# Optimization experiments

Measured on AMD Instinct MI355X. Metric: run time of the kernel, lower is better.

The kernel has to match this reference:

```python
import jax, jax.numpy as jnp
import numpy as np

D_MODEL = 528
N_HEADS = 16
FEAT = 16           # feature_dim
HEAD_DIM = 33       # d_model // num_heads == 2*FEAT + 1 (required by the module's math)
WINDOW = 64
EPS = 1e-9


def setup_inputs() -> dict:
    key = jax.random.key(0)
    ks = jax.random.split(key, 10)
    B, S = 2, 2048
    hidden_states = jax.random.normal(ks[0], (B, S, D_MODEL), dtype=jnp.float32)
    attention_mask = jnp.ones((B, S), dtype=jnp.int32)
    sc = 0.02
    # weights stored as (in, out); torch Linear applies x @ W.T so this is the transposed weight
    Wq_lin = jax.random.normal(ks[1], (D_MODEL, FEAT * N_HEADS), dtype=jnp.float32) * sc
    Wk_lin = jax.random.normal(ks[2], (D_MODEL, FEAT * N_HEADS), dtype=jnp.float32) * sc
    Wv_lin = jax.random.normal(ks[3], (D_MODEL, HEAD_DIM * N_HEADS), dtype=jnp.float32) * sc
    Wo_lin = jax.random.normal(ks[4], (HEAD_DIM * N_HEADS, D_MODEL), dtype=jnp.float32) * sc
    Wq_win = jax.random.normal(ks[5], (D_MODEL, D_MODEL), dtype=jnp.float32) * sc
    Wk_win = jax.random.normal(ks[6], (D_MODEL, D_MODEL), dtype=jnp.float32) * sc
    Wv_win = jax.random.normal(ks[7], (D_MODEL, D_MODEL), dtype=jnp.float32) * sc
    Wo_win = jax.random.normal(ks[8], (D_MODEL, D_MODEL), dtype=jnp.float32) * sc
    return {
        "hidden_states": hidden_states,
        "attention_mask": attention_mask,
        "Wq_lin": Wq_lin, "Wk_lin": Wk_lin, "Wv_lin": Wv_lin, "Wo_lin": Wo_lin,
        "Wq_win": Wq_win, "Wk_win": Wk_win, "Wv_win": Wv_win, "Wo_win": Wo_win,
    }


def _linear_attention(x, mask, Wq, Wk, Wv, Wo):
    B, S, _ = x.shape
    q = (x @ Wq).reshape(B, S, N_HEADS, FEAT).transpose(0, 2, 1, 3)      # bhsf
    k = (x @ Wk).reshape(B, S, N_HEADS, FEAT).transpose(0, 2, 1, 3)
    v = (x @ Wv).reshape(B, S, N_HEADS, HEAD_DIM).transpose(0, 2, 1, 3)  # bhse
    # Taylor feature map: [1, q, 0.5*q^2] -> feature dim 2*FEAT+1 == HEAD_DIM
    qe = jnp.concatenate([jnp.ones_like(q[..., :1]), q, 0.5 * q * q], axis=-1)
    ke = jnp.concatenate([jnp.ones_like(k[..., :1]), k, 0.5 * k * k], axis=-1)
    kv = jnp.einsum('bhnd,bhne->bhde', ke, v)          # (B,H,Dexp,HEAD_DIM)
    qkv = jnp.einsum('bhnd,bhde->bhne', qe, kv)        # (B,H,S,HEAD_DIM)
    # z[b,h,n,e] = (sum_d qe[b,h,n,d]) * ksum[b,h,e]  (faithful to torch einsum with size-1 n)
    z = qe.sum(-1, keepdims=True) * ke.sum(2, keepdims=True)  # (B,H,S,Dexp==HEAD_DIM)
    out = qkv / (z + EPS)
    out = jnp.where((mask == 0)[:, None, :, None], 0.0, out)
    out = out.transpose(0, 2, 1, 3).reshape(B, S, N_HEADS * HEAD_DIM)
    return out @ Wo


def _window_attention(x, mask, Wq, Wk, Wv, Wo):
    B, S, _ = x.shape
    q = (x @ Wq).reshape(B, S, N_HEADS, HEAD_DIM).transpose(0, 2, 1, 3)
    k = (x @ Wk).reshape(B, S, N_HEADS, HEAD_DIM).transpose(0, 2, 1, 3)
    v = (x @ Wv).reshape(B, S, N_HEADS, HEAD_DIM).transpose(0, 2, 1, 3)
    scores = jnp.einsum('bhnd,bhmd->bhnm', q, k) / np.sqrt(HEAD_DIM).astype(np.float32)
    # tril(diagonal=window_size-1): allow key index m <= n + WINDOW - 1
    i = jnp.arange(S)[:, None]
    j = jnp.arange(S)[None, :]
    band = (j <= i + WINDOW - 1)
    neg_inf = jnp.asarray(-jnp.inf, scores.dtype)
    scores = jnp.where(band[None, None], scores, neg_inf)
    scores = jnp.where((mask == 0)[:, None, None, :], neg_inf, scores)
    attn = jax.nn.softmax(scores, axis=-1)
    out = jnp.einsum('bhnm,bhmd->bhnd', attn, v)
    out = out.transpose(0, 2, 1, 3).reshape(B, S, D_MODEL)
    return out @ Wo


def reference(hidden_states, attention_mask,
              Wq_lin, Wk_lin, Wv_lin, Wo_lin,
              Wq_win, Wk_win, Wv_win, Wo_win):
    lin = _linear_attention(hidden_states, attention_mask, Wq_lin, Wk_lin, Wv_lin, Wo_lin)
    win = _window_attention(hidden_states, attention_mask, Wq_win, Wk_win, Wv_win, Wo_win)
    return lin + win
```

## Files before the change

### kernel.cpp

```cpp
#include <hip/hip_runtime.h>

#define NH 16
#define FEAT 16
#define HD 33
#define DM 528
#define WIN 64
#define EPSF 1e-9f
#define K1C (0.17407765595569785f * 1.4426950408889634f)
#define KP 544
#define KSPLIT 1632
#define NPROJ 2112
#define KOUT 1056
#define OPS 4352
#define NCH 16
#define ZPARTS 4

typedef float f32x4 __attribute__((ext_vector_type(4)));
typedef short short8 __attribute__((ext_vector_type(8)));

__device__ inline ushort f2bf(float f) {
  uint u = __float_as_uint(f);
  uint r = u + 0x7fffu + ((u >> 16) & 1u);
  return (ushort)(r >> 16);
}
__device__ inline ushort f2bf_tr(float f) { return (ushort)(__float_as_uint(f) >> 16); }
__device__ inline float bf2f(ushort u) { return __uint_as_float(((uint)u) << 16); }

__global__ __launch_bounds__(256) void prep_all(const float* __restrict__ x,
                                                const float* __restrict__ Wq_lin,
                                                const float* __restrict__ Wk_lin,
                                                const float* __restrict__ Wv_lin,
                                                const float* __restrict__ Wo_lin,
                                                const float* __restrict__ Wq_win,
                                                const float* __restrict__ Wk_win,
                                                const float* __restrict__ Wv_win,
                                                const float* __restrict__ Wo_win,
                                                ushort* __restrict__ xhi,
                                                ushort* __restrict__ xlo,
                                                ushort* __restrict__ Wqks,
                                                ushort* __restrict__ WprojT,
                                                ushort* __restrict__ WoT2, int M) {
  const int stride = gridDim.x * 256;
  const int tid0 = blockIdx.x * 256 + threadIdx.x;
  for (int j = tid0; j < M * 68; j += stride) {
    int row = j / 68, c8 = (j - row * 68) * 8;
    short8 h8, l8;
    if (c8 < DM) {
      float4 f0 = *(const float4*)&x[(size_t)row * DM + c8];
      float4 f1 = *(const float4*)&x[(size_t)row * DM + c8 + 4];
      float vv[8] = {f0.x, f0.y, f0.z, f0.w, f1.x, f1.y, f1.z, f1.w};
#pragma unroll
      for (int z = 0; z < 8; ++z) {
        ushort h = f2bf(vv[z]);
        h8[z] = (short)h;
        l8[z] = (short)f2bf(vv[z] - bf2f(h));
      }
    } else {
      h8 = (short8){0, 0, 0, 0, 0, 0, 0, 0};
      l8 = h8;
    }
    *(short8*)&xhi[(size_t)row * KP + c8] = h8;
    *(short8*)&xlo[(size_t)row * KP + c8] = l8;
  }
  for (int i = tid0; i < 512 * KSPLIT; i += stride) {
    int n = i / KSPLIT, kp = i - n * KSPLIT;
    int seg = kp / KP, kk = kp - seg * KP;
    float v = 0.f;
    if (kk < DM) v = (n < 256) ? Wq_lin[(size_t)kk * 256 + n] : Wk_lin[(size_t)kk * 256 + (n - 256)];
    ushort h = f2bf(v);
    if (seg == 2) h = f2bf(v - bf2f(h));
    Wqks[i] = h;
  }
  for (int i = tid0; i < NPROJ * KP; i += stride) {
    int n = i / KP, k = i - n * KP;
    float v = 0.f;
    if (k < DM) {
      if (n < DM) v = Wq_win[(size_t)k * DM + n];
      else if (n < 2 * DM) v = Wk_win[(size_t)k * DM + (n - DM)] * K1C;
      else if (n < 3 * DM) v = Wv_win[(size_t)k * DM + (n - 2 * DM)];
      else v = Wv_lin[(size_t)k * DM + (n - 3 * DM)];
    }
    WprojT[i] = f2bf(v);
  }
  for (int i = tid0; i < DM * KOUT; i += stride) {
    int n = i / KOUT, k = i - n * KOUT;
    float v = (k < DM) ? Wo_lin[(size_t)k * DM + n] : Wo_win[(size_t)(k - DM) * DM + n];
    WoT2[i] = f2bf(v);
  }
}

__global__ __launch_bounds__(256) void proj_fused(const ushort* __restrict__ xhi,
                                                  const ushort* __restrict__ xlo,
                                                  const ushort* __restrict__ Wqks,
                                                  const ushort* __restrict__ WprojT,
                                                  float* __restrict__ qk,
                                                  ushort* __restrict__ qkvw,
                                                  float* __restrict__ v_lin,
                                                  const int* __restrict__ maskp,
                                                  int S) {
  __shared__ ushort As[128][36];
  __shared__ ushort Bs[128][36];
  const int bm = blockIdx.x * 128;
  const int tid = threadIdx.x;
  const int lane = tid & 63, w = tid >> 6;
  const int lo = lane & 15, hi = lane >> 4;
  const int wr = w >> 1, wc = w & 1;
  const short8 zv = {0, 0, 0, 0, 0, 0, 0, 0};
  f32x4 acc[4][4];
#pragma unroll
  for (int mb = 0; mb < 4; ++mb)
#pragma unroll
    for (int nb = 0; nb < 4; ++nb) acc[mb][nb] = (f32x4){0.f, 0.f, 0.f, 0.f};

  if (blockIdx.y < 17) {
    const int bn = blockIdx.y * 128;
    for (int k0 = 0; k0 < KP; k0 += 32) {
      short8 a_ld[2], b_ld[2];
#pragma unroll
      for (int p = 0; p < 2; ++p) {
        int c = tid + p * 256;
        int row = c >> 2, cc = c & 3;
        a_ld[p] = *(const short8*)&xhi[(size_t)(bm + row) * KP + k0 + cc * 8];
        int bnr = bn + row;
        b_ld[p] = (bnr < NPROJ) ? *(const short8*)&WprojT[(size_t)bnr * KP + k0 + cc * 8] : zv;
      }
      __syncthreads();
#pragma unroll
      for (int p = 0; p < 2; ++p) {
        int c = tid + p * 256;
        int row = c >> 2, cc = c & 3;
        *(short8*)&As[row][cc * 8] = a_ld[p];
        *(short8*)&Bs[row][cc * 8] = b_ld[p];
      }
      __syncthreads();
      short8 afr[4], bfr[4];
#pragma unroll
      for (int mb = 0; mb < 4; ++mb) afr[mb] = *(const short8*)&As[wr * 64 + 16 * mb + lo][8 * hi];
#pragma unroll
      for (int nb = 0; nb < 4; ++nb) bfr[nb] = *(const short8*)&Bs[wc * 64 + 16 * nb + lo][8 * hi];
#pragma unroll
      for (int mb = 0; mb < 4; ++mb)
#pragma unroll
        for (int nb = 0; nb < 4; ++nb)
          acc[mb][nb] = __builtin_amdgcn_mfma_f32_16x16x32_bf16(afr[mb], bfr[nb], acc[mb][nb], 0, 0, 0);
    }
#pragma unroll
    for (int nb = 0; nb < 4; ++nb) {
      const int col = bn + wc * 64 + 16 * nb + lo;
      if (col >= NPROJ) continue;
      const int seg = col / DM;
      const int cc = col - seg * DM;
      if (seg == 3) {
#pragma unroll
        for (int mb = 0; mb < 4; ++mb)
#pragma unroll
          for (int r = 0; r < 4; ++r) {
            int row = bm + wr * 64 + 16 * mb + 4 * hi + r;
            v_lin[(size_t)row * DM + cc] = acc[mb][nb][r];
          }
      } else {
        const uint h = ((uint)cc * 993u) >> 15;
        const int e = cc - (int)h * 33;
        ushort* dst = qkvw + (size_t)seg * (32u * (uint)S * 40u);
#pragma unroll
        for (int mb = 0; mb < 4; ++mb)
#pragma unroll
          for (int r = 0; r < 4; ++r) {
            int row = bm + wr * 64 + 16 * mb + 4 * hi + r;
            int b = (row >= S) ? 1 : 0;
            int nn = row - b * S;
            float val = acc[mb][nb][r];
            if (seg == 2) {
              size_t tb = (size_t)(b * NH + (int)h) * 40;
              dst[(tb + e) * S + nn] = f2bf(val);
              if (e == 0) {
                dst[(tb + 33) * S + nn] = 0x3F80;
#pragma unroll
                for (int z = 34; z < 40; ++z) dst[(tb + z) * S + nn] = 0;
              }
            } else {
              size_t base = ((size_t)(b * NH + (int)h) * S + nn) * 40;
              dst[base + e] = f2bf(val);
              if (e == 0) {
                ushort pad33 = (seg == 0) ? (ushort)0x3F80
                                          : (maskp[row] ? (ushort)0 : f2bf(-1e30f));
                dst[base + 33] = pad33;
#pragma unroll
                for (int z = 34; z < 40; ++z) dst[base + z] = 0;
              }
            }
          }
      }
    }
  } else {
    const int bn = (blockIdx.y - 17) * 128;
    for (int k0 = 0; k0 < KSPLIT; k0 += 32) {
      const int seg = k0 / KP;
      const int kk = k0 - seg * KP;
      const ushort* xsrc = (seg == 1) ? xlo : xhi;
      short8 a_ld[2], b_ld[2];
#pragma unroll
      for (int p = 0; p < 2; ++p) {
        int c = tid + p * 256;
        int row = c >> 2, cc = c & 3;
        a_ld[p] = *(const short8*)&xsrc[(size_t)(bm + row) * KP + kk + cc * 8];
        b_ld[p] = *(const short8*)&Wqks[(size_t)(bn + row) * KSPLIT + k0 + cc * 8];
      }
      __syncthreads();
#pragma unroll
      for (int p = 0; p < 2; ++p) {
        int c = tid + p * 256;
        int row = c >> 2, cc = c & 3;
        *(short8*)&As[row][cc * 8] = a_ld[p];
        *(short8*)&Bs[row][cc * 8] = b_ld[p];
      }
      __syncthreads();
      short8 afr[4], bfr[4];
#pragma unroll
      for (int mb = 0; mb < 4; ++mb) afr[mb] = *(const short8*)&As[wr * 64 + 16 * mb + lo][8 * hi];
#pragma unroll
      for (int nb = 0; nb < 4; ++nb) bfr[nb] = *(const short8*)&Bs[wc * 64 + 16 * nb + lo][8 * hi];
#pragma unroll
      for (int mb = 0; mb < 4; ++mb)
#pragma unroll
        for (int nb = 0; nb < 4; ++nb)
          acc[mb][nb] = __builtin_amdgcn_mfma_f32_16x16x32_bf16(afr[mb], bfr[nb], acc[mb][nb], 0, 0, 0);
    }
#pragma unroll
    for (int mb = 0; mb < 4; ++mb)
#pragma unroll
      for (int nb = 0; nb < 4; ++nb) {
        int col = bn + wc * 64 + 16 * nb + lo;
#pragma unroll
        for (int r = 0; r < 4; ++r) {
          int row = bm + wr * 64 + 16 * mb + 4 * hi + r;
          qk[(size_t)row * 512 + col] = acc[mb][nb][r];
        }
      }
  }
}

__global__ __launch_bounds__(256) void gemm_out(const ushort* __restrict__ A,
                                                const ushort* __restrict__ Bt,
                                                float* __restrict__ C, int S) {
  __shared__ ushort As[128][36];
  __shared__ ushort Bs[128][36];
  const int bm = blockIdx.x * 128, bn = blockIdx.y * 128;
  const int tid = threadIdx.x;
  const int lane = tid & 63, w = tid >> 6;
  const int lo = lane & 15, hi = lane >> 4;
  const int wr = w >> 1, wc = w & 1;
  f32x4 acc[4][4];
#pragma unroll
  for (int mb = 0; mb < 4; ++mb)
#pragma unroll
    for (int nb = 0; nb < 4; ++nb) acc[mb][nb] = (f32x4){0.f, 0.f, 0.f, 0.f};
  const short8 zv = {0, 0, 0, 0, 0, 0, 0, 0};

  for (int k0 = 0; k0 < KOUT; k0 += 32) {
    short8 a_ld[2], b_ld[2];
#pragma unroll
    for (int p = 0; p < 2; ++p) {
      int c = tid + p * 256;
      int row = c >> 2, cc = c & 3;
      a_ld[p] = *(const short8*)&A[(size_t)(bm + row) * KOUT + k0 + cc * 8];
      int bnr = bn + row;
      b_ld[p] = (bnr < DM) ? *(const short8*)&Bt[(size_t)bnr * KOUT + k0 + cc * 8] : zv;
    }
    __syncthreads();
#pragma unroll
    for (int p = 0; p < 2; ++p) {
      int c = tid + p * 256;
      int row = c >> 2, cc = c & 3;
      *(short8*)&As[row][cc * 8] = a_ld[p];
      *(short8*)&Bs[row][cc * 8] = b_ld[p];
    }
    __syncthreads();
    short8 afr[4], bfr[4];
#pragma unroll
    for (int mb = 0; mb < 4; ++mb) afr[mb] = *(const short8*)&As[wr * 64 + 16 * mb + lo][8 * hi];
#pragma unroll
    for (int nb = 0; nb < 4; ++nb) bfr[nb] = *(const short8*)&Bs[wc * 64 + 16 * nb + lo][8 * hi];
#pragma unroll
    for (int mb = 0; mb < 4; ++mb)
#pragma unroll
      for (int nb = 0; nb < 4; ++nb)
        acc[mb][nb] = __builtin_amdgcn_mfma_f32_16x16x32_bf16(afr[mb], bfr[nb], acc[mb][nb], 0, 0, 0);
  }
#pragma unroll
  for (int nb = 0; nb < 4; ++nb) {
    const int col = bn + wc * 64 + 16 * nb + lo;
    if (col >= DM) continue;
#pragma unroll
    for (int mb = 0; mb < 4; ++mb)
#pragma unroll
      for (int r = 0; r < 4; ++r) {
        int row = bm + wr * 64 + 16 * mb + 4 * hi + r;
        C[(size_t)row * DM + col] = acc[mb][nb][r];
      }
  }
}

__global__ __launch_bounds__(256) void lin_red(const float* __restrict__ kvp,
                                               float* __restrict__ kvr) {
  int bh = blockIdx.x;
  for (int i = threadIdx.x; i < 1188; i += 256) {
    float s = 0.f;
#pragma unroll
    for (int c = 0; c < NCH; ++c) s += kvp[(size_t)(bh * NCH + c) * 1188 + i];
    kvr[(size_t)bh * 1188 + i] = s;
  }
}

__global__ __launch_bounds__(256) void win_kv(const ushort* __restrict__ qwb,
                                              const ushort* __restrict__ kwb,
                                              const ushort* __restrict__ vwbT,
                                              ushort* __restrict__ Opart,
                                              const float* __restrict__ qk,
                                              const float* __restrict__ v_lin,
                                              float* __restrict__ kvp,
                                              int B, int S, int NT2) {
  __shared__ ushort sh[4][32][72];
  const int tid = threadIdx.x;
  const int NWINBLK = NT2 * 32 * ZPARTS;
  const int bx = blockIdx.x;

  if (bx < NWINBLK) {
    const int bh = bx & 31;
    const int qp = bx >> 5;
    const int part = qp / NT2;
    const int qt = NT2 - 1 - (qp - part * NT2);
    const int NT = NT2 * 2;
    const int T = min(NT, 2 * qt + 3);
    if (part >= T) return;
    const int n0 = qt * 128;
    const int lane = tid & 63, w = tid >> 6;
    const int lo = lane & 15, hi = lane >> 4;
    const short8 zv = {0, 0, 0, 0, 0, 0, 0, 0};
    ushort (*Ps)[32][72] = sh;

    short8 qf[2][2];
#pragma unroll
    for (int qr = 0; qr < 2; ++qr) {
      const ushort* qrow = qwb + ((size_t)bh * S + n0 + w * 32 + qr * 16 + lo) * 40;
      qf[qr][0] = *(const short8*)&qrow[8 * hi];
      qf[qr][1] = (hi == 0) ? *(const short8*)&qrow[32] : zv;
    }

    const ushort* kb = kwb + (size_t)bh * S * 40;
    const ushort* vb = vwbT + (size_t)bh * 40 * S;
    int evc[3];
#pragma unroll
    for (int eb = 0; eb < 3; ++eb) {
      int e = 16 * eb + lo;
      evc[eb] = (e > 39) ? 39 : e;
    }

    f32x4 Oacc[2][3];
#pragma unroll
    for (int qr = 0; qr < 2; ++qr)
#pragma unroll
      for (int eb = 0; eb < 3; ++eb) Oacc[qr][eb] = (f32x4){0.f, 0.f, 0.f, 0.f};

    for (int t = part; t < T; t += ZPARTS) {
      const int m0 = t * 64;
      short8 kf0[4], kf1[4];
#pragma unroll
      for (int bb = 0; bb < 4; ++bb) {
        const ushort* kr = kb + (size_t)(m0 + 16 * bb + lo) * 40;
        kf0[bb] = *(const short8*)&kr[8 * hi];
        kf1[bb] = *(const short8*)&kr[32];
      }
      short8 vf0[3], vf1[3];
#pragma unroll
      for (int eb = 0; eb < 3; ++eb) {
        const ushort* vr = vb + (size_t)evc[eb] * S + m0;
        vf0[eb] = *(const short8*)&vr[8 * hi];
        vf1[eb] = *(const short8*)&vr[32 + 8 * hi];
      }

      f32x4 accS[2][4];
#pragma unroll
      for (int qr = 0; qr < 2; ++qr)
#pragma unroll
        for (int bb = 0; bb < 4; ++bb) accS[qr][bb] = (f32x4){0.f, 0.f, 0.f, 0.f};
      __builtin_amdgcn_s_setprio(1);
#pragma unroll
      for (int bb = 0; bb < 4; ++bb)
#pragma unroll
        for (int qr = 0; qr < 2; ++qr) {
          accS[qr][bb] = __builtin_amdgcn_mfma_f32_16x16x32_bf16(qf[qr][0], kf0[bb], accS[qr][bb], 0, 0, 0);
          accS[qr][bb] = __builtin_amdgcn_mfma_f32_16x16x32_bf16(qf[qr][1], kf1[bb], accS[qr][bb], 0, 0, 0);
        }
      __builtin_amdgcn_s_setprio(0);

      const bool boundary = (m0 > n0);
      const int dmn = m0 - n0;
#pragma unroll
      for (int qr = 0; qr < 2; ++qr)
#pragma unroll
        for (int bb = 0; bb < 4; ++bb)
#pragma unroll
          for (int r = 0; r < 4; ++r) {
            float p = exp2f(accS[qr][bb][r]);
            if (boundary) {
              int rr = w * 32 + qr * 16 + 4 * hi + r;
              int c = 16 * bb + lo;
              if (c > rr + 63 - dmn) p = 0.f;
            }
            Ps[w][qr * 16 + 4 * hi + r][16 * bb + lo] = f2bf_tr(p);
          }

      __builtin_amdgcn_s_setprio(1);
#pragma unroll
      for (int qr = 0; qr < 2; ++qr) {
        short8 pf0 = *(const short8*)&Ps[w][qr * 16 + lo][8 * hi];
        short8 pf1 = *(const short8*)&Ps[w][qr * 16 + lo][32 + 8 * hi];
#pragma unroll
        for (int eb = 0; eb < 3; ++eb) {
          Oacc[qr][eb] = __builtin_amdgcn_mfma_f32_16x16x32_bf16(pf0, vf0[eb], Oacc[qr][eb], 0, 0, 0);
          Oacc[qr][eb] = __builtin_amdgcn_mfma_f32_16x16x32_bf16(pf1, vf1[eb], Oacc[qr][eb], 0, 0, 0);
        }
      }
      __builtin_amdgcn_s_setprio(0);
    }

    const size_t ob = ((size_t)(bh * NT2 + qt) * ZPARTS + part) * OPS;
#pragma unroll
    for (int qr = 0; qr < 2; ++qr)
#pragma unroll
      for (int eb = 0; eb < 3; ++eb) {
        int e = 16 * eb + lo;
        if (e < 34) {
#pragma unroll
          for (int r = 0; r < 4; ++r)
            Opart[ob + (size_t)(w * 32 + qr * 16 + 4 * hi + r) * 34 + e] = f2bf(Oacc[qr][eb][r]);
        }
      }
  } else {
    const int idx = bx - NWINBLK;
    const int bh = idx & 31, chunk = idx >> 5;
    const int b = bh >> 4, h = bh & 15;
    float* kraw = (float*)sh;
    float* vsh = kraw + 64 * 17;
    if (tid < 64) { vsh[tid * 36 + 33] = 1.f; vsh[tid * 36 + 34] = 0.f; vsh[tid * 36 + 35] = 0.f; }
    f32x4 acc0 = {0.f, 0.f, 0.f, 0.f}, acc1 = {0.f, 0.f, 0.f, 0.f};
    const int d0 = tid / 9, c40 = (tid % 9) * 4;
    const int idx1 = tid + 256;
    const int d1 = idx1 / 9, c41 = (idx1 % 9) * 4;
    const int SC = S / NCH;
    const int nbeg = chunk * SC;
    __syncthreads();
    for (int n0 = nbeg; n0 < nbeg + SC; n0 += 64) {
      {
        int row = tid >> 2, f4 = (tid & 3) * 4;
        float4 kv4 = *(const float4*)&qk[(size_t)(b * S + n0 + row) * 512 + 256 + h * 16 + f4];
        kraw[row * 17 + f4 + 0] = kv4.x; kraw[row * 17 + f4 + 1] = kv4.y;
        kraw[row * 17 + f4 + 2] = kv4.z; kraw[row * 17 + f4 + 3] = kv4.w;
      }
      for (int i = tid; i < 64 * 33; i += 256) {
        int n = i / 33, e = i - n * 33;
        vsh[n * 36 + e] = v_lin[(size_t)(b * S + n0 + n) * DM + h * HD + e];
      }
      __syncthreads();
#pragma unroll 4
      for (int n = 0; n < 64; ++n) {
        {
          float ke;
          if (d0 == 0) ke = 1.f;
          else if (d0 < 17) ke = kraw[n * 17 + d0 - 1];
          else { float kk = kraw[n * 17 + d0 - 17]; ke = 0.5f * kk * kk; }
          f32x4 v = *(const f32x4*)&vsh[n * 36 + c40];
          acc0 += ke * v;
        }
        if (idx1 < 297) {
          float ke;
          if (d1 < 17) ke = kraw[n * 17 + d1 - 1];
          else { float kk = kraw[n * 17 + d1 - 17]; ke = 0.5f * kk * kk; }
          f32x4 v = *(const f32x4*)&vsh[n * 36 + c41];
          acc1 += ke * v;
        }
      }
      __syncthreads();
    }
    float* dst = kvp + (size_t)(bh * NCH + chunk) * 1188;
    *(f32x4*)&dst[d0 * 36 + c40] = acc0;
    if (idx1 < 297) *(f32x4*)&dst[d1 * 36 + c41] = acc1;
  }
}

__global__ __launch_bounds__(256) void comb_lin(const ushort* __restrict__ Opart,
                                                const float* __restrict__ qk,
                                                const float* __restrict__ kvr,
                                                const int* __restrict__ mask,
                                                ushort* __restrict__ cat,
                                                int B, int S, int NT2) {
  __shared__ float shf[160];
  const int tid = threadIdx.x;
  const int NCOMB = NT2 * 32;
  const int bx = blockIdx.x;

  if (bx < NCOMB) {
    const int bh = bx & 31;
    const int qt = bx >> 5;
    const int b = bh >> 4, h = bh & 15;
    const int T = min(NT2 * 2, 2 * qt + 3);
    const int P = min(ZPARTS, T);
    const size_t base = (size_t)(bh * NT2 + qt) * ZPARTS * OPS;
    float* linv = shf;
    if (tid < 128) {
      float l = 0.f;
      for (int p = 0; p < P; ++p) l += bf2f(Opart[base + (size_t)p * OPS + tid * 34 + 33]);
      linv[tid] = (l > 0.f) ? 1.f / l : 0.f;
    }
    __syncthreads();
    for (int i = tid; i < 128 * 33; i += 256) {
      int row = i / 33, e = i - row * 33;
      float o = 0.f;
      for (int p = 0; p < P; ++p) o += bf2f(Opart[base + (size_t)p * OPS + row * 34 + e]);
      int n = qt * 128 + row;
      cat[((size_t)(b * S + n)) * KOUT + DM + h * HD + e] = f2bf(o * linv[row]);
    }
  } else {
    const int bs = bx - NCOMB;
    const int b = (bs >= S) ? 1 : 0;
    float* qsh = shf;
    __shared__ float qsh2[NH * 17];
    qsh = qsh2;
    for (int i = tid; i < NH * FEAT; i += 256)
      qsh[(i >> 4) * 17 + (i & 15)] = qk[(size_t)bs * 512 + i];
    __syncthreads();
    const int msk = mask[bs];
    for (int o = tid; o < DM; o += 256) {
      uint h = ((uint)o * 993u) >> 15;
      int e = o - (int)h * 33;
      const float* kvh = kvr + (size_t)(b * NH + (int)h) * 1188;
      float qsum = 1.f, qkv = kvh[e];
#pragma unroll
      for (int f = 0; f < FEAT; ++f) {
        float q = qsh[h * 17 + f];
        float q2 = 0.5f * q * q;
        qsum += q + q2;
        qkv += q * kvh[(1 + f) * 36 + e] + q2 * kvh[(17 + f) * 36 + e];
      }
      float z = qsum * kvh[e * 36 + 33];
      float outv = qkv / (z + EPSF);
      if (msk == 0) outv = 0.f;
      cat[(size_t)bs * KOUT + o] = f2bf(outv);
    }
  }
}

extern "C" void kernel_launch(void* const* d_in, const int* in_sizes, int n_in,
                              void* d_out, int out_size, void* d_ws, size_t ws_size,
                              hipStream_t stream) {
  const float* x      = (const float*)d_in[0];
  const int*   mask   = (const int*)d_in[1];
  const float* Wq_lin = (const float*)d_in[2];
  const float* Wk_lin = (const float*)d_in[3];
  const float* Wv_lin = (const float*)d_in[4];
  const float* Wo_lin = (const float*)d_in[5];
  const float* Wq_win = (const float*)d_in[6];
  const float* Wk_win = (const float*)d_in[7];
  const float* Wv_win = (const float*)d_in[8];
  const float* Wo_win = (const float*)d_in[9];
  float* out = (float*)d_out;

  const int BS = in_sizes[1];
  const int B = 2;
  const int S = BS / B;
  const int NT2 = S / 128;
  const int M = BS;

  float* ws = (float*)d_ws;
  float* qk      = ws;  ws += (size_t)BS * 512;
  float* v_lin   = ws;  ws += (size_t)BS * DM;
  float* kvp     = ws;  ws += (size_t)B * NH * NCH * 1188;
  float* kvr     = ws;  ws += (size_t)B * NH * 1188;
  ushort* ub     = (ushort*)ws;
  ushort* x_hi   = ub;  ub += (size_t)M * KP;
  ushort* x_lo   = ub;  ub += (size_t)M * KP;
  ushort* qkvw   = ub;  ub += (size_t)3 * 32 * S * 40;
  ushort* cat    = ub;  ub += (size_t)M * KOUT;
  ushort* WprojT = ub;  ub += (size_t)NPROJ * KP;
  ushort* WoT2   = ub;  ub += (size_t)DM * KOUT;
  ushort* Wqks   = ub;  ub += (size_t)512 * KSPLIT;
  ushort* Opart  = ub;  ub += (size_t)32 * NT2 * ZPARTS * OPS;

  ushort* qwb  = qkvw;
  ushort* kwb  = qkvw + (size_t)32 * S * 40;
  ushort* vwbT = qkvw + (size_t)64 * S * 40;

  dim3 blk(256);

  prep_all<<<2048, blk, 0, stream>>>(x, Wq_lin, Wk_lin, Wv_lin, Wo_lin,
                                     Wq_win, Wk_win, Wv_win, Wo_win,
                                     x_hi, x_lo, Wqks, WprojT, WoT2, M);

  proj_fused<<<dim3(M / 128, 21), blk, 0, stream>>>(x_hi, x_lo, Wqks, WprojT,
                                                    qk, qkvw, v_lin, mask, S);

  win_kv<<<dim3(NT2 * 32 * ZPARTS + B * NH * NCH), blk, 0, stream>>>(
      qwb, kwb, vwbT, Opart, qk, v_lin, kvp, B, S, NT2);

  lin_red<<<dim3(B * NH), blk, 0, stream>>>(kvp, kvr);

  comb_lin<<<dim3(NT2 * 32 + BS), blk, 0, stream>>>(Opart, qk, kvr, mask, cat, B, S, NT2);

  gemm_out<<<dim3(M / 128, (DM + 127) / 128), blk, 0, stream>>>(cat, WoT2, out, S);
}
```

Baseline: 193.1 us.

## Split-K the q/k projection with atomics, halve window parts, double-buffer K/V loads

The linear-attention q/k projection, which previously looped over all three bf16 split segments in one block, is now split across three grid rows per segment. Each row accumulates its result into qk with atomicAdd, and prep_all zeroes qk first. The window kernel drops from four to two key-tile partitions per query tile and software-pipelines the K/V fragment loads with two register buffers, so the next tile loads while the current one computes. The aim is more parallelism in the projection and hidden load latency in the window kernel. The cost is atomic traffic, higher register pressure, and fewer window blocks.

Result: no change. 192.6 us (-0.3%).

```diff
diff --git a/kernel.cpp b/kernel.cpp
--- a/kernel.cpp
+++ b/kernel.cpp
@@ -13,7 +13,7 @@
 #define KOUT 1056
 #define OPS 4352
 #define NCH 16
-#define ZPARTS 4
+#define ZPARTS 2
 
 typedef float f32x4 __attribute__((ext_vector_type(4)));
 typedef short short8 __attribute__((ext_vector_type(8)));
@@ -39,7 +39,8 @@
                                                 ushort* __restrict__ xlo,
                                                 ushort* __restrict__ Wqks,
                                                 ushort* __restrict__ WprojT,
-                                                ushort* __restrict__ WoT2, int M) {
+                                                ushort* __restrict__ WoT2,
+                                                float* __restrict__ qk, int M) {
   const int stride = gridDim.x * 256;
   const int tid0 = blockIdx.x * 256 + threadIdx.x;
   for (int j = tid0; j < M * 68; j += stride) {
@@ -62,6 +63,8 @@
     *(short8*)&xhi[(size_t)row * KP + c8] = h8;
     *(short8*)&xlo[(size_t)row * KP + c8] = l8;
   }
+  for (int i = tid0; i < M * 128; i += stride)
+    ((float4*)qk)[i] = make_float4(0.f, 0.f, 0.f, 0.f);
   for (int i = tid0; i < 512 * KSPLIT; i += stride) {
     int n = i / KSPLIT, kp = i - n * KSPLIT;
     int seg = kp / KP, kk = kp - seg * KP;
@@ -193,18 +196,19 @@
       }
     }
   } else {
-    const int bn = (blockIdx.y - 17) * 128;
-    for (int k0 = 0; k0 < KSPLIT; k0 += 32) {
-      const int seg = k0 / KP;
-      const int kk = k0 - seg * KP;
-      const ushort* xsrc = (seg == 1) ? xlo : xhi;
+    const int yy = blockIdx.y - 17;
+    const int seg = yy >> 2;
+    const int bn = (yy & 3) * 128;
+    const ushort* xsrc = (seg == 1) ? xlo : xhi;
+    const int kb = seg * KP;
+    for (int k0 = 0; k0 < KP; k0 += 32) {
       short8 a_ld[2], b_ld[2];
 #pragma unroll
       for (int p = 0; p < 2; ++p) {
         int c = tid + p * 256;
         int row = c >> 2, cc = c & 3;
-        a_ld[p] = *(const short8*)&xsrc[(size_t)(bm + row) * KP + kk + cc * 8];
-        b_ld[p] = *(const short8*)&Wqks[(size_t)(bn + row) * KSPLIT + k0 + cc * 8];
+        a_ld[p] = *(const short8*)&xsrc[(size_t)(bm + row) * KP + k0 + cc * 8];
+        b_ld[p] = *(const short8*)&Wqks[(size_t)(bn + row) * KSPLIT + kb + k0 + cc * 8];
       }
       __syncthreads();
 #pragma unroll
@@ -234,7 +238,7 @@
 #pragma unroll
         for (int r = 0; r < 4; ++r) {
           int row = bm + wr * 64 + 16 * mb + 4 * hi + r;
-          qk[(size_t)row * 512 + col] = acc[mb][nb][r];
+          atomicAdd(&qk[(size_t)row * 512 + col], acc[mb][nb][r]);
         }
       }
   }
@@ -362,23 +366,26 @@
 #pragma unroll
       for (int eb = 0; eb < 3; ++eb) Oacc[qr][eb] = (f32x4){0.f, 0.f, 0.f, 0.f};
 
-    for (int t = part; t < T; t += ZPARTS) {
-      const int m0 = t * 64;
-      short8 kf0[4], kf1[4];
+    auto LOADT = [&](short8 (&K0)[4], short8 (&K1)[4],
+                     short8 (&V0)[3], short8 (&V1)[3], int tt) {
+      const int m0 = tt * 64;
 #pragma unroll
       for (int bb = 0; bb < 4; ++bb) {
         const ushort* kr = kb + (size_t)(m0 + 16 * bb + lo) * 40;
-        kf0[bb] = *(const short8*)&kr[8 * hi];
-        kf1[bb] = *(const short8*)&kr[32];
-      }
-      short8 vf0[3], vf1[3];
+        K0[bb] = *(const short8*)&kr[8 * hi];
+        K1[bb] = *(const short8*)&kr[32];
+      }
 #pragma unroll
       for (int eb = 0; eb < 3; ++eb) {
         const ushort* vr = vb + (size_t)evc[eb] * S + m0;
-        vf0[eb] = *(const short8*)&vr[8 * hi];
-        vf1[eb] = *(const short8*)&vr[32 + 8 * hi];
-      }
-
+        V0[eb] = *(const short8*)&vr[8 * hi];
+        V1[eb] = *(const short8*)&vr[32 + 8 * hi];
+      }
+    };
+
+    auto CTILE = [&](short8 (&K0)[4], short8 (&K1)[4],
+                     short8 (&V0)[3], short8 (&V1)[3], int tt) {
+      const int m0 = tt * 64;
       f32x4 accS[2][4];
 #pragma unroll
       for (int qr = 0; qr < 2; ++qr)
@@ -389,11 +396,10 @@
       for (int bb = 0; bb < 4; ++bb)
 #pragma unroll
         for (int qr = 0; qr < 2; ++qr) {
-          accS[qr][bb] = __builtin_amdgcn_mfma_f32_16x16x32_bf16(qf[qr][0], kf0[bb], accS[qr][bb], 0, 0, 0);
-          accS[qr][bb] = __builtin_amdgcn_mfma_f32_16x16x32_bf16(qf[qr][1], kf1[bb], accS[qr][bb], 0, 0, 0);
+          accS[qr][bb] = __builtin_amdgcn_mfma_f32_16x16x32_bf16(qf[qr][0], K0[bb], accS[qr][bb], 0, 0, 0);
+          accS[qr][bb] = __builtin_amdgcn_mfma_f32_16x16x32_bf16(qf[qr][1], K1[bb], accS[qr][bb], 0, 0, 0);
         }
       __builtin_amdgcn_s_setprio(0);
-
       const bool boundary = (m0 > n0);
       const int dmn = m0 - n0;
 #pragma unroll
@@ -410,7 +416,6 @@
             }
             Ps[w][qr * 16 + 4 * hi + r][16 * bb + lo] = f2bf_tr(p);
           }
-
       __builtin_amdgcn_s_setprio(1);
 #pragma unroll
       for (int qr = 0; qr < 2; ++qr) {
@@ -418,11 +423,30 @@
         short8 pf1 = *(const short8*)&Ps[w][qr * 16 + lo][32 + 8 * hi];
 #pragma unroll
         for (int eb = 0; eb < 3; ++eb) {
-          Oacc[qr][eb] = __builtin_amdgcn_mfma_f32_16x16x32_bf16(pf0, vf0[eb], Oacc[qr][eb], 0, 0, 0);
-          Oacc[qr][eb] = __builtin_amdgcn_mfma_f32_16x16x32_bf16(pf1, vf1[eb], Oacc[qr][eb], 0, 0, 0);
+          Oacc[qr][eb] = __builtin_amdgcn_mfma_f32_16x16x32_bf16(pf0, V0[eb], Oacc[qr][eb], 0, 0, 0);
+          Oacc[qr][eb] = __builtin_amdgcn_mfma_f32_16x16x32_bf16(pf1, V1[eb], Oacc[qr][eb], 0, 0, 0);
         }
       }
       __builtin_amdgcn_s_setprio(0);
+    };
+
+    short8 kf0A[4], kf1A[4], vf0A[3], vf1A[3];
+    short8 kf0B[4], kf1B[4], vf0B[3], vf1B[3];
+    int t = part;
+    LOADT(kf0A, kf1A, vf0A, vf1A, t);
+    for (;;) {
+      int tn = t + ZPARTS;
+      bool hn = tn < T;
+      if (hn) LOADT(kf0B, kf1B, vf0B, vf1B, tn);
+      CTILE(kf0A, kf1A, vf0A, vf1A, t);
+      if (!hn) break;
+      t = tn;
+      tn = t + ZPARTS;
+      hn = tn < T;
+      if (hn) LOADT(kf0A, kf1A, vf0A, vf1A, tn);
+      CTILE(kf0B, kf1B, vf0B, vf1B, t);
+      if (!hn) break;
+      t = tn;
     }
 
     const size_t ob = ((size_t)(bh * NT2 + qt) * ZPARTS + part) * OPS;
@@ -524,9 +548,8 @@
   } else {
     const int bs = bx - NCOMB;
     const int b = (bs >= S) ? 1 : 0;
-    float* qsh = shf;
     __shared__ float qsh2[NH * 17];
-    qsh = qsh2;
+    float* qsh = qsh2;
     for (int i = tid; i < NH * FEAT; i += 256)
       qsh[(i >> 4) * 17 + (i & 15)] = qk[(size_t)bs * 512 + i];
     __syncthreads();
@@ -595,9 +618,9 @@
 
   prep_all<<<2048, blk, 0, stream>>>(x, Wq_lin, Wk_lin, Wv_lin, Wo_lin,
                                      Wq_win, Wk_win, Wv_win, Wo_win,
-                                     x_hi, x_lo, Wqks, WprojT, WoT2, M);
-
-  proj_fused<<<dim3(M / 128, 21), blk, 0, stream>>>(x_hi, x_lo, Wqks, WprojT,
+                                     x_hi, x_lo, Wqks, WprojT, WoT2, qk, M);
+
+  proj_fused<<<dim3(M / 128, 29), blk, 0, stream>>>(x_hi, x_lo, Wqks, WprojT,
                                                     qk, qkvw, v_lin, mask, S);
 
   win_kv<<<dim3(NT2 * 32 * ZPARTS + B * NH * NCH), blk, 0, stream>>>(
```
